# Kernel optimization log

Measured on AMD Instinct MI355X. Metric: run time of the kernel, lower is better.

## Reference

```python
import jax, jax.numpy as jnp
import numpy as np
import math

N_HEAD = 16
NEG = -1e30  # stands in for -inf in masked_fill; identical post-softmax


def setup_inputs() -> dict:
    key = jax.random.key(0)
    ks = jax.random.split(key, 8)
    B, S, D = 4, 2048, 1024
    x = jax.random.normal(ks[0], (B, S, D), dtype=jnp.float32)
    mask = jax.random.randint(ks[1], (B, S), 0, 2).astype(jnp.int32)
    qmask = jax.random.randint(ks[2], (B, S), 0, 2).astype(jnp.int32)
    w_qkv = jax.random.normal(ks[3], (3 * D, D), dtype=jnp.float32) / math.sqrt(D)
    w_fc = jax.random.normal(ks[4], (D, D), dtype=jnp.float32) / math.sqrt(D)
    b_fc = jax.random.normal(ks[5], (D,), dtype=jnp.float32) * 0.01
    # shift = abs(randn)+0.001 (positive), bias = -abs(randn) (negative)
    shift = jnp.abs(jax.random.normal(ks[6], (1,), dtype=jnp.float32)) + 0.001
    bias_p = -jnp.abs(jax.random.normal(ks[7], (1,), dtype=jnp.float32))
    return {"x": x, "mask": mask, "qmask": qmask, "use_Gaussian": 1,
            "w_qkv": w_qkv, "w_fc": w_fc, "b_fc": b_fc,
            "shift": shift, "bias_p": bias_p}


def reference(x, mask, qmask, use_Gaussian, w_qkv, w_fc, b_fc, shift, bias_p):
    B, S, D = x.shape
    H = N_HEAD
    Dh = D // H
    scale = math.sqrt(Dh)
    qkv = jnp.einsum('bsd,ed->bse', x, w_qkv)  # [B,S,3D]
    q, k, v = jnp.split(qkv, 3, axis=-1)
    q = q.reshape(B, S, H, Dh).transpose(0, 2, 1, 3)  # [B,H,S,Dh]
    k = k.reshape(B, S, H, Dh).transpose(0, 2, 1, 3)
    v = v.reshape(B, S, H, Dh).transpose(0, 2, 1, 3)
    attn = jnp.einsum('bhqd,bhkd->bhqk', q, k) / scale
    key_mask = (mask != 0)[:, None, None, :]  # [B,1,1,S]
    attn = jnp.where(key_mask, attn, NEG)
    if use_Gaussian:
        idx = jnp.arange(S, dtype=jnp.float32)
        sq_dist = (idx[:, None] - idx[None, :]) ** 2  # (i-j)^2 == H+H.T-2G
        dis = -(shift[0] * sq_dist + bias_p[0])  # [S,S]
        attn = attn + dis[None, None]
    attn = jax.nn.softmax(attn, axis=-1)
    out = jnp.einsum('bhqk,bhkd->bhqd', attn, v)
    out = out.transpose(0, 2, 1, 3).reshape(B, S, D)
    return jnp.einsum('bsd,ed->bse', out, w_fc) + b_fc
```

## Files before the change

### kernel.cpp

```cpp
#include <hip/hip_runtime.h>
#include <stdint.h>
#include <math.h>

#define DI __device__ __forceinline__

typedef unsigned short u16;
typedef __bf16   bf16x8 __attribute__((ext_vector_type(8)));
typedef float    f32x4  __attribute__((ext_vector_type(4)));

#define BSZ 4
#define SEQ 2048
#define DMODEL 1024
#define NHEAD 16
#define DHEAD 64

DI u16 f2b(float f) {
    uint32_t u = __float_as_uint(f);
    u += 0x7fffu + ((u >> 16) & 1u);
    return (u16)(u >> 16);
}

DI void async16(const void* g, void* l) {
    __builtin_amdgcn_global_load_lds(
        (const __attribute__((address_space(1))) void*)g,
        (__attribute__((address_space(3))) void*)l, 16, 0, 0);
}

__global__ __launch_bounds__(256) void cast_all(
    const float* __restrict__ x,  const float* __restrict__ wq,
    const float* __restrict__ wf, u16* __restrict__ xb,
    u16* __restrict__ wqb, u16* __restrict__ wfb)
{
    const int idx = blockIdx.x * 256 + threadIdx.x;
    const float* src; u16* dst; int off;
    if (idx < 2097152)      { src = x;  dst = xb;  off = idx; }
    else if (idx < 2883584) { src = wq; dst = wqb; off = idx - 2097152; }
    else                    { src = wf; dst = wfb; off = idx - 2883584; }
    const int i = off * 4;
    f32x4 v = *(const f32x4*)(src + i);
    uint32_t lo = (uint32_t)f2b(v[0]) | ((uint32_t)f2b(v[1]) << 16);
    uint32_t hi = (uint32_t)f2b(v[2]) | ((uint32_t)f2b(v[3]) << 16);
    *(uint2*)(dst + i) = make_uint2(lo, hi);
}

template <int MODE>
__global__ __launch_bounds__(256) void gemm_bt(
    const u16* __restrict__ A, const u16* __restrict__ Bm, int K,
    u16* __restrict__ qb, u16* __restrict__ kb, u16* __restrict__ vb,
    const float* __restrict__ bias, float* __restrict__ outF, int N)
{
    __shared__ u16 As[128 * 64];
    __shared__ u16 Bs[128 * 64];

    const int tid  = threadIdx.x;
    const int l    = tid & 63, w = tid >> 6;
    const int quad = l >> 4, lc = l & 15;
    const int wm   = w >> 1, wn = w & 1;
    const int m0   = blockIdx.y * 128, n0 = blockIdx.x * 128;

    f32x4 acc[4][4];
#pragma unroll
    for (int i = 0; i < 4; i++)
#pragma unroll
        for (int j = 0; j < 4; j++) acc[i][j] = (f32x4){0.f, 0.f, 0.f, 0.f};

    const int  srow   = tid >> 3;
    const int  schunk = (tid & 7) ^ (srow & 7);
    const size_t aBase = (size_t)(m0 + srow) * K + schunk * 8;
    const size_t bBase = (size_t)(n0 + srow) * K + schunk * 8;

    for (int k0 = 0; k0 < K; k0 += 64) {
        __syncthreads();
#pragma unroll
        for (int i = 0; i < 4; i++) {
            async16(A  + aBase + (size_t)(32 * i) * K + k0, As + i * 2048 + w * 512);
            async16(Bm + bBase + (size_t)(32 * i) * K + k0, Bs + i * 2048 + w * 512);
        }
        __syncthreads();

#pragma unroll
        for (int kh = 0; kh < 2; kh++) {
            bf16x8 af[4], bf[4];
            const int g = kh * 4 + quad;
#pragma unroll
            for (int mi = 0; mi < 4; mi++) {
                const int mr = wm * 64 + mi * 16 + lc;
                af[mi] = *(const bf16x8*)&As[mr * 64 + ((g ^ (mr & 7)) * 8)];
            }
#pragma unroll
            for (int ni = 0; ni < 4; ni++) {
                const int nr = wn * 64 + ni * 16 + lc;
                bf[ni] = *(const bf16x8*)&Bs[nr * 64 + ((g ^ (nr & 7)) * 8)];
            }
#pragma unroll
            for (int mi = 0; mi < 4; mi++)
#pragma unroll
                for (int ni = 0; ni < 4; ni++)
                    acc[mi][ni] = __builtin_amdgcn_mfma_f32_16x16x32_bf16(
                        af[mi], bf[ni], acc[mi][ni], 0, 0, 0);
        }
    }

#pragma unroll
    for (int mi = 0; mi < 4; mi++) {
        const int mrow = m0 + wm * 64 + mi * 16 + quad * 4;
#pragma unroll
        for (int ni = 0; ni < 4; ni++) {
            const int e = n0 + wn * 64 + ni * 16 + lc;
#pragma unroll
            for (int r = 0; r < 4; r++) {
                const int m = mrow + r;
                const float v = acc[mi][ni][r];
                if (MODE == 0) {
                    const int part = e >> 10, rem = e & 1023;
                    const int h = rem >> 6, dh = rem & 63;
                    const int b = m >> 11, s = m & 2047;
                    u16* dst = (part == 0) ? qb : ((part == 1) ? kb : vb);
                    dst[(((size_t)(b * NHEAD + h) * SEQ + s) << 6) + dh] = f2b(v);
                } else {
                    outF[(size_t)m * N + e] = v + bias[e];
                }
            }
        }
    }
}

#define PST 72
__global__ __launch_bounds__(256) void attn_kernel(
    const u16* __restrict__ Q, const u16* __restrict__ Kg, const u16* __restrict__ Vg,
    const int* __restrict__ mask, const int* __restrict__ gaussp,
    const float* __restrict__ shiftp, const float* __restrict__ biaspp,
    u16* __restrict__ outA)
{
    __shared__ u16 Ks[8 * 64 * 8];
    __shared__ u16 Vt[64 * PST];
    __shared__ u16 Ps[4 * 32 * PST];

    const int tid  = threadIdx.x;
    const int l    = tid & 63, w = tid >> 6;
    const int quad = l >> 4, lc = l & 15;
    const int qt = blockIdx.x, h = blockIdx.y, b = blockIdx.z;
    const int bh = b * NHEAD + h;
    const int q0 = qt * 128;

    const float shift = shiftp[0];
    const float biasp = biaspp[0];
    const int   gauss = gaussp[0];

    const u16* Qbase = Q  + ((size_t)bh * SEQ << 6);
    const u16* Kbase = Kg + ((size_t)bh * SEQ << 6);
    const u16* Vbase = Vg + ((size_t)bh * SEQ << 6);
    const int* mbase = mask + b * SEQ;

    int kt_lo = 0, kt_hi = SEQ / 64 - 1;
    if (gauss) {
        const int dwin = (int)__fsqrt_rn(30.0f / shift) + 1;
        int lo = q0 - dwin;          if (lo < 0) lo = 0;
        int hi = q0 + 127 + dwin;    if (hi > SEQ - 1) hi = SEQ - 1;
        kt_lo = lo >> 6;
        kt_hi = hi >> 6;
    }

    bf16x8 qf[2][2];
#pragma unroll
    for (int mi = 0; mi < 2; mi++)
#pragma unroll
        for (int ks = 0; ks < 2; ks++)
            qf[mi][ks] = *(const bf16x8*)(Qbase +
                ((size_t)(q0 + w * 32 + mi * 16 + lc) << 6) + ks * 32 + quad * 8);

    f32x4 oacc[2][4];
#pragma unroll
    for (int mi = 0; mi < 2; mi++)
#pragma unroll
        for (int dt = 0; dt < 4; dt++) oacc[mi][dt] = (f32x4){0.f, 0.f, 0.f, 0.f};
    float lsum[2][4];
#pragma unroll
    for (int mi = 0; mi < 2; mi++)
#pragma unroll
        for (int r = 0; r < 4; r++) lsum[mi][r] = 0.f;

    for (int kt = kt_lo; kt <= kt_hi; ++kt) {
        const int kk0 = kt * 64;
        __syncthreads();

        async16(Kbase + (size_t)(kk0 + l) * 64 + w * 8,       Ks + w * 512);
        async16(Kbase + (size_t)(kk0 + l) * 64 + (4 + w) * 8, Ks + 2048 + w * 512);

        {
            const u16* vg = Vbase + (size_t)(kk0 + l) * 64 + w * 16;
            bf16x8 v0 = *(const bf16x8*)vg;
            bf16x8 v1 = *(const bf16x8*)(vg + 8);
            const u16* v0b = (const u16*)&v0;
            const u16* v1b = (const u16*)&v1;
#pragma unroll
            for (int j = 0; j < 8; j++) Vt[(w * 16 + j) * PST + l] = v0b[j];
#pragma unroll
            for (int j = 0; j < 8; j++) Vt[(w * 16 + 8 + j) * PST + l] = v1b[j];
        }
        __syncthreads();

        bf16x8 kf[4][2];
#pragma unroll
        for (int nt = 0; nt < 4; nt++)
#pragma unroll
            for (int ks = 0; ks < 2; ks++)
                kf[nt][ks] = *(const bf16x8*)&Ks[(ks * 4 + quad) * 512 + (nt * 16 + lc) * 8];

        f32x4 sf[2][4];
#pragma unroll
        for (int mi = 0; mi < 2; mi++)
#pragma unroll
            for (int nt = 0; nt < 4; nt++) sf[mi][nt] = (f32x4){0.f, 0.f, 0.f, 0.f};
#pragma unroll
        for (int mi = 0; mi < 2; mi++)
#pragma unroll
            for (int nt = 0; nt < 4; nt++)
#pragma unroll
                for (int ks = 0; ks < 2; ks++)
                    sf[mi][nt] = __builtin_amdgcn_mfma_f32_16x16x32_bf16(
                        qf[mi][ks], kf[nt][ks], sf[mi][nt], 0, 0, 0);

        float madd[4]; float jj[4];
#pragma unroll
        for (int nt = 0; nt < 4; nt++) {
            const int j = kk0 + nt * 16 + lc;
            madd[nt] = mbase[j] ? 0.f : -1e30f;
            jj[nt] = (float)j;
        }
#pragma unroll
        for (int mi = 0; mi < 2; mi++) {
#pragma unroll
            for (int r = 0; r < 4; r++) {
                const float fi = (float)(q0 + w * 32 + mi * 16 + quad * 4 + r);
                float psum = 0.f;
#pragma unroll
                for (int nt = 0; nt < 4; nt++) {
                    float s = sf[mi][nt][r] * 0.125f + madd[nt] - 8.0f;
                    if (gauss) { const float d = fi - jj[nt]; s -= shift * d * d + biasp; }
                    const float p = __expf(s);
                    psum += p;
                    Ps[(w * 32 + mi * 16 + quad * 4 + r) * PST + nt * 16 + lc] = f2b(p);
                }
                lsum[mi][r] += psum;
            }
        }

        bf16x8 pa[2][2], vf[4][2];
#pragma unroll
        for (int mi = 0; mi < 2; mi++)
#pragma unroll
            for (int ks = 0; ks < 2; ks++)
                pa[mi][ks] = *(const bf16x8*)&Ps[(w * 32 + mi * 16 + lc) * PST + ks * 32 + quad * 8];
#pragma unroll
        for (int dt = 0; dt < 4; dt++)
#pragma unroll
            for (int ks = 0; ks < 2; ks++)
                vf[dt][ks] = *(const bf16x8*)&Vt[(dt * 16 + lc) * PST + ks * 32 + quad * 8];
#pragma unroll
        for (int mi = 0; mi < 2; mi++)
#pragma unroll
            for (int dt = 0; dt < 4; dt++)
#pragma unroll
                for (int ks = 0; ks < 2; ks++)
                    oacc[mi][dt] = __builtin_amdgcn_mfma_f32_16x16x32_bf16(
                        pa[mi][ks], vf[dt][ks], oacc[mi][dt], 0, 0, 0);
    }

    float lrow[2][4];
#pragma unroll
    for (int mi = 0; mi < 2; mi++)
#pragma unroll
        for (int r = 0; r < 4; r++) {
            float ts = lsum[mi][r];
            ts += __shfl_xor(ts, 1);
            ts += __shfl_xor(ts, 2);
            ts += __shfl_xor(ts, 4);
            ts += __shfl_xor(ts, 8);
            lrow[mi][r] = ts;
        }

#pragma unroll
    for (int mi = 0; mi < 2; mi++)
#pragma unroll
        for (int dt = 0; dt < 4; dt++)
#pragma unroll
            for (int r = 0; r < 4; r++) {
                const int qg  = q0 + w * 32 + mi * 16 + quad * 4 + r;
                const int col = h * 64 + dt * 16 + lc;
                const float v = oacc[mi][dt][r] / lrow[mi][r];
                outA[((size_t)(b * SEQ + qg) << 10) + col] = f2b(v);
            }
}

extern "C" void kernel_launch(void* const* d_in, const int* in_sizes, int n_in,
                              void* d_out, int out_size, void* d_ws, size_t ws_size,
                              hipStream_t stream)
{
    const float* x      = (const float*)d_in[0];
    const int*   mask   = (const int*)d_in[1];
    const int*   gaussp = (const int*)d_in[3];
    const float* w_qkv  = (const float*)d_in[4];
    const float* w_fc   = (const float*)d_in[5];
    const float* b_fc   = (const float*)d_in[6];
    const float* shiftp = (const float*)d_in[7];
    const float* biaspp = (const float*)d_in[8];
    float* out = (float*)d_out;

    char* ws = (char*)d_ws;
    u16* xb  = (u16*)(ws);
    u16* wqb = (u16*)(ws + 16777216);
    u16* wfb = (u16*)(ws + 23068672);
    u16* qb  = (u16*)(ws + 25165824);
    u16* kb  = (u16*)(ws + 41943040);
    u16* vb  = (u16*)(ws + 58720256);

    cast_all<<<12288, 256, 0, stream>>>(x, w_qkv, w_fc, xb, wqb, wfb);

    gemm_bt<0><<<dim3(24, 64), 256, 0, stream>>>(xb, wqb, DMODEL,
                                                 qb, kb, vb, nullptr, nullptr, 3 * DMODEL);

    attn_kernel<<<dim3(SEQ / 128, NHEAD, BSZ), 256, 0, stream>>>(
        qb, kb, vb, mask, gaussp, shiftp, biaspp, xb);

    gemm_bt<1><<<dim3(8, 64), 256, 0, stream>>>(xb, wfb, DMODEL,
                                                nullptr, nullptr, nullptr, b_fc, out, DMODEL);
}
```

Before: 226.2 us.

## Split-K output GEMM with atomics, halve attention query tile, packed bf16 casts

The output projection GEMM is split along K into two halves. Each half atomically adds its partial sums into an output buffer that the cast kernel now pre-fills with the bias, which doubles the block count on the small 8x64 grid. The attention kernel moves from 128 to 64 query rows per block, giving twice as many blocks and fewer registers per wave, and it computes a tighter Gaussian window. Float-to-bf16 conversion now uses the packed HIP intrinsic. In exchange, the kernel pays atomic traffic, a non-deterministic summation order, and reloads K/V tiles for each smaller query tile.

```diff
diff --git a/kernel.cpp b/kernel.cpp
--- a/kernel.cpp
+++ b/kernel.cpp
@@ -1,4 +1,5 @@
 #include <hip/hip_runtime.h>
+#include <hip/hip_bf16.h>
 #include <stdint.h>
 #include <math.h>
 
@@ -20,6 +21,11 @@
     return (u16)(u >> 16);
 }
 
+DI uint32_t f2b2(float a, float b) {
+    __hip_bfloat162 h = __float22bfloat162_rn(float2{a, b});
+    uint32_t u; __builtin_memcpy(&u, &h, 4); return u;
+}
+
 DI void async16(const void* g, void* l) {
     __builtin_amdgcn_global_load_lds(
         (const __attribute__((address_space(1))) void*)g,
@@ -28,26 +34,30 @@
 
 __global__ __launch_bounds__(256) void cast_all(
     const float* __restrict__ x,  const float* __restrict__ wq,
-    const float* __restrict__ wf, u16* __restrict__ xb,
-    u16* __restrict__ wqb, u16* __restrict__ wfb)
+    const float* __restrict__ wf, const float* __restrict__ bias,
+    u16* __restrict__ xb, u16* __restrict__ wqb, u16* __restrict__ wfb,
+    float* __restrict__ outF)
 {
     const int idx = blockIdx.x * 256 + threadIdx.x;
+    if (idx >= 3145728) {
+        const int off = idx - 3145728;
+        *(f32x4*)(outF + off * 4) = *(const f32x4*)(bias + (off & 255) * 4);
+        return;
+    }
     const float* src; u16* dst; int off;
     if (idx < 2097152)      { src = x;  dst = xb;  off = idx; }
     else if (idx < 2883584) { src = wq; dst = wqb; off = idx - 2097152; }
     else                    { src = wf; dst = wfb; off = idx - 2883584; }
     const int i = off * 4;
     f32x4 v = *(const f32x4*)(src + i);
-    uint32_t lo = (uint32_t)f2b(v[0]) | ((uint32_t)f2b(v[1]) << 16);
-    uint32_t hi = (uint32_t)f2b(v[2]) | ((uint32_t)f2b(v[3]) << 16);
-    *(uint2*)(dst + i) = make_uint2(lo, hi);
-}
-
-template <int MODE>
+    *(uint2*)(dst + i) = make_uint2(f2b2(v[0], v[1]), f2b2(v[2], v[3]));
+}
+
+template <int MODE, int KS>
 __global__ __launch_bounds__(256) void gemm_bt(
     const u16* __restrict__ A, const u16* __restrict__ Bm, int K,
     u16* __restrict__ qb, u16* __restrict__ kb, u16* __restrict__ vb,
-    const float* __restrict__ bias, float* __restrict__ outF, int N)
+    float* __restrict__ outF, int N)
 {
     __shared__ u16 As[128 * 64];
     __shared__ u16 Bs[128 * 64];
@@ -57,6 +67,8 @@
     const int quad = l >> 4, lc = l & 15;
     const int wm   = w >> 1, wn = w & 1;
     const int m0   = blockIdx.y * 128, n0 = blockIdx.x * 128;
+    const int kb0  = (MODE == 1) ? blockIdx.z * KS : 0;
+    const int kb1  = (MODE == 1) ? kb0 + KS : K;
 
     f32x4 acc[4][4];
 #pragma unroll
@@ -69,7 +81,7 @@
     const size_t aBase = (size_t)(m0 + srow) * K + schunk * 8;
     const size_t bBase = (size_t)(n0 + srow) * K + schunk * 8;
 
-    for (int k0 = 0; k0 < K; k0 += 64) {
+    for (int k0 = kb0; k0 < kb1; k0 += 64) {
         __syncthreads();
 #pragma unroll
         for (int i = 0; i < 4; i++) {
@@ -118,7 +130,7 @@
                     u16* dst = (part == 0) ? qb : ((part == 1) ? kb : vb);
                     dst[(((size_t)(b * NHEAD + h) * SEQ + s) << 6) + dh] = f2b(v);
                 } else {
-                    outF[(size_t)m * N + e] = v + bias[e];
+                    atomicAdd(&outF[(size_t)m * N + e], v);
                 }
             }
         }
@@ -134,14 +146,14 @@
 {
     __shared__ u16 Ks[8 * 64 * 8];
     __shared__ u16 Vt[64 * PST];
-    __shared__ u16 Ps[4 * 32 * PST];
+    __shared__ u16 Ps[64 * PST];
 
     const int tid  = threadIdx.x;
     const int l    = tid & 63, w = tid >> 6;
     const int quad = l >> 4, lc = l & 15;
     const int qt = blockIdx.x, h = blockIdx.y, b = blockIdx.z;
     const int bh = b * NHEAD + h;
-    const int q0 = qt * 128;
+    const int q0 = qt * 64;
 
     const float shift = shiftp[0];
     const float biasp = biaspp[0];
@@ -156,29 +168,23 @@
     if (gauss) {
         const int dwin = (int)__fsqrt_rn(30.0f / shift) + 1;
         int lo = q0 - dwin;          if (lo < 0) lo = 0;
-        int hi = q0 + 127 + dwin;    if (hi > SEQ - 1) hi = SEQ - 1;
+        int hi = q0 + 63 + dwin;     if (hi > SEQ - 1) hi = SEQ - 1;
         kt_lo = lo >> 6;
         kt_hi = hi >> 6;
     }
 
-    bf16x8 qf[2][2];
-#pragma unroll
-    for (int mi = 0; mi < 2; mi++)
-#pragma unroll
-        for (int ks = 0; ks < 2; ks++)
-            qf[mi][ks] = *(const bf16x8*)(Qbase +
-                ((size_t)(q0 + w * 32 + mi * 16 + lc) << 6) + ks * 32 + quad * 8);
-
-    f32x4 oacc[2][4];
-#pragma unroll
-    for (int mi = 0; mi < 2; mi++)
-#pragma unroll
-        for (int dt = 0; dt < 4; dt++) oacc[mi][dt] = (f32x4){0.f, 0.f, 0.f, 0.f};
-    float lsum[2][4];
-#pragma unroll
-    for (int mi = 0; mi < 2; mi++)
-#pragma unroll
-        for (int r = 0; r < 4; r++) lsum[mi][r] = 0.f;
+    bf16x8 qf[2];
+#pragma unroll
+    for (int ks = 0; ks < 2; ks++)
+        qf[ks] = *(const bf16x8*)(Qbase +
+            ((size_t)(q0 + w * 16 + lc) << 6) + ks * 32 + quad * 8);
+
+    f32x4 oacc[4];
+#pragma unroll
+    for (int dt = 0; dt < 4; dt++) oacc[dt] = (f32x4){0.f, 0.f, 0.f, 0.f};
+    float lsum[4];
+#pragma unroll
+    for (int r = 0; r < 4; r++) lsum[r] = 0.f;
 
     for (int kt = kt_lo; kt <= kt_hi; ++kt) {
         const int kk0 = kt * 64;
@@ -207,19 +213,15 @@
             for (int ks = 0; ks < 2; ks++)
                 kf[nt][ks] = *(const bf16x8*)&Ks[(ks * 4 + quad) * 512 + (nt * 16 + lc) * 8];
 
-        f32x4 sf[2][4];
-#pragma unroll
-        for (int mi = 0; mi < 2; mi++)
-#pragma unroll
-            for (int nt = 0; nt < 4; nt++) sf[mi][nt] = (f32x4){0.f, 0.f, 0.f, 0.f};
-#pragma unroll
-        for (int mi = 0; mi < 2; mi++)
-#pragma unroll
-            for (int nt = 0; nt < 4; nt++)
-#pragma unroll
-                for (int ks = 0; ks < 2; ks++)
-                    sf[mi][nt] = __builtin_amdgcn_mfma_f32_16x16x32_bf16(
-                        qf[mi][ks], kf[nt][ks], sf[mi][nt], 0, 0, 0);
+        f32x4 sf[4];
+#pragma unroll
+        for (int nt = 0; nt < 4; nt++) sf[nt] = (f32x4){0.f, 0.f, 0.f, 0.f};
+#pragma unroll
+        for (int nt = 0; nt < 4; nt++)
+#pragma unroll
+            for (int ks = 0; ks < 2; ks++)
+                sf[nt] = __builtin_amdgcn_mfma_f32_16x16x32_bf16(
+                    qf[ks], kf[nt][ks], sf[nt], 0, 0, 0);
 
         float madd[4]; float jj[4];
 #pragma unroll
@@ -229,68 +231,60 @@
             jj[nt] = (float)j;
         }
 #pragma unroll
-        for (int mi = 0; mi < 2; mi++) {
-#pragma unroll
-            for (int r = 0; r < 4; r++) {
-                const float fi = (float)(q0 + w * 32 + mi * 16 + quad * 4 + r);
-                float psum = 0.f;
-#pragma unroll
-                for (int nt = 0; nt < 4; nt++) {
-                    float s = sf[mi][nt][r] * 0.125f + madd[nt] - 8.0f;
-                    if (gauss) { const float d = fi - jj[nt]; s -= shift * d * d + biasp; }
-                    const float p = __expf(s);
-                    psum += p;
-                    Ps[(w * 32 + mi * 16 + quad * 4 + r) * PST + nt * 16 + lc] = f2b(p);
-                }
-                lsum[mi][r] += psum;
+        for (int r = 0; r < 4; r++) {
+            const float fi = (float)(q0 + w * 16 + quad * 4 + r);
+            float p[4];
+#pragma unroll
+            for (int nt = 0; nt < 4; nt++) {
+                float s = sf[nt][r] * 0.125f + madd[nt] - 8.0f;
+                if (gauss) { const float d = fi - jj[nt]; s -= shift * d * d + biasp; }
+                p[nt] = __expf(s);
             }
-        }
-
-        bf16x8 pa[2][2], vf[4][2];
-#pragma unroll
-        for (int mi = 0; mi < 2; mi++)
-#pragma unroll
-            for (int ks = 0; ks < 2; ks++)
-                pa[mi][ks] = *(const bf16x8*)&Ps[(w * 32 + mi * 16 + lc) * PST + ks * 32 + quad * 8];
+            lsum[r] += (p[0] + p[1]) + (p[2] + p[3]);
+            const uint32_t p01 = f2b2(p[0], p[1]);
+            const uint32_t p23 = f2b2(p[2], p[3]);
+            u16* prow = &Ps[(w * 16 + quad * 4 + r) * PST + lc];
+            prow[0]  = (u16)p01;  prow[16] = (u16)(p01 >> 16);
+            prow[32] = (u16)p23;  prow[48] = (u16)(p23 >> 16);
+        }
+
+        bf16x8 pa[2], vf[4][2];
+#pragma unroll
+        for (int ks = 0; ks < 2; ks++)
+            pa[ks] = *(const bf16x8*)&Ps[(w * 16 + lc) * PST + ks * 32 + quad * 8];
 #pragma unroll
         for (int dt = 0; dt < 4; dt++)
 #pragma unroll
             for (int ks = 0; ks < 2; ks++)
                 vf[dt][ks] = *(const bf16x8*)&Vt[(dt * 16 + lc) * PST + ks * 32 + quad * 8];
 #pragma unroll
-        for (int mi = 0; mi < 2; mi++)
-#pragma unroll
-            for (int dt = 0; dt < 4; dt++)
-#pragma unroll
-                for (int ks = 0; ks < 2; ks++)
-                    oacc[mi][dt] = __builtin_amdgcn_mfma_f32_16x16x32_bf16(
-                        pa[mi][ks], vf[dt][ks], oacc[mi][dt], 0, 0, 0);
-    }
-
-    float lrow[2][4];
-#pragma unroll
-    for (int mi = 0; mi < 2; mi++)
+        for (int dt = 0; dt < 4; dt++)
+#pragma unroll
+            for (int ks = 0; ks < 2; ks++)
+                oacc[dt] = __builtin_amdgcn_mfma_f32_16x16x32_bf16(
+                    pa[ks], vf[dt][ks], oacc[dt], 0, 0, 0);
+    }
+
+    float lrow[4];
+#pragma unroll
+    for (int r = 0; r < 4; r++) {
+        float ts = lsum[r];
+        ts += __shfl_xor(ts, 1);
+        ts += __shfl_xor(ts, 2);
+        ts += __shfl_xor(ts, 4);
+        ts += __shfl_xor(ts, 8);
+        lrow[r] = ts;
+    }
+
+#pragma unroll
+    for (int dt = 0; dt < 4; dt++)
 #pragma unroll
         for (int r = 0; r < 4; r++) {
-            float ts = lsum[mi][r];
-            ts += __shfl_xor(ts, 1);
-            ts += __shfl_xor(ts, 2);
-            ts += __shfl_xor(ts, 4);
-            ts += __shfl_xor(ts, 8);
-            lrow[mi][r] = ts;
-        }
-
-#pragma unroll
-    for (int mi = 0; mi < 2; mi++)
-#pragma unroll
-        for (int dt = 0; dt < 4; dt++)
-#pragma unroll
-            for (int r = 0; r < 4; r++) {
-                const int qg  = q0 + w * 32 + mi * 16 + quad * 4 + r;
-                const int col = h * 64 + dt * 16 + lc;
-                const float v = oacc[mi][dt][r] / lrow[mi][r];
-                outA[((size_t)(b * SEQ + qg) << 10) + col] = f2b(v);
-            }
+            const int qg  = q0 + w * 16 + quad * 4 + r;
+            const int col = h * 64 + dt * 16 + lc;
+            const float v = oacc[dt][r] / lrow[r];
+            outA[((size_t)(b * SEQ + qg) << 10) + col] = f2b(v);
+        }
 }
 
 extern "C" void kernel_launch(void* const* d_in, const int* in_sizes, int n_in,
@@ -315,14 +309,14 @@
     u16* kb  = (u16*)(ws + 41943040);
     u16* vb  = (u16*)(ws + 58720256);
 
-    cast_all<<<12288, 256, 0, stream>>>(x, w_qkv, w_fc, xb, wqb, wfb);
-
-    gemm_bt<0><<<dim3(24, 64), 256, 0, stream>>>(xb, wqb, DMODEL,
-                                                 qb, kb, vb, nullptr, nullptr, 3 * DMODEL);
-
-    attn_kernel<<<dim3(SEQ / 128, NHEAD, BSZ), 256, 0, stream>>>(
+    cast_all<<<20480, 256, 0, stream>>>(x, w_qkv, w_fc, b_fc, xb, wqb, wfb, out);
+
+    gemm_bt<0, 1024><<<dim3(24, 64), 256, 0, stream>>>(
+        xb, wqb, DMODEL, qb, kb, vb, nullptr, 3 * DMODEL);
+
+    attn_kernel<<<dim3(SEQ / 64, NHEAD, BSZ), 256, 0, stream>>>(
         qb, kb, vb, mask, gaussp, shiftp, biaspp, xb);
 
-    gemm_bt<1><<<dim3(8, 64), 256, 0, stream>>>(xb, wfb, DMODEL,
-                                                nullptr, nullptr, nullptr, b_fc, out, DMODEL);
-}
+    gemm_bt<1, 512><<<dim3(8, 64, 2), 256, 0, stream>>>(
+        xb, wfb, DMODEL, nullptr, nullptr, nullptr, out, DMODEL);
+}
```

After: 266.0 us. 1.18x slower.
